# Kernel tuning notes

Hardware: AMD Instinct MI355X
Metric: run time of the kernel (lower is better)

The kernel has to match this reference:

```python
import jax, jax.numpy as jnp
import numpy as np

H, DH = 16, 64  # heads, dim_head (inner_dim = 1024)


def _sdpa(q, k, v):
    # q: (B, Q, D), k/v: (B, K, D); scale = 1/sqrt(D) as in F.scaled_dot_product_attention
    scale = 1.0 / jnp.sqrt(jnp.asarray(q.shape[-1], q.dtype))
    s = jnp.einsum('bqd,bkd->bqk', q, k) * scale
    return jnp.einsum('bqk,bkd->bqd', jax.nn.softmax(s, axis=-1), v)


def setup_inputs() -> dict:
    key = jax.random.key(0)
    ks = jax.random.split(key, 3)
    b, f, n, dim = 8, 16, 196, 1024
    N = 1 + f * n  # CLS + frames*patches = 3137
    x = jax.random.normal(ks[0], (b, N, dim), jnp.float32)
    w_qkv = jax.random.normal(ks[1], (3 * H * DH, dim), jnp.float32) * 0.02
    w_out = jax.random.normal(ks[2], (dim, H * DH), jnp.float32) * 0.02
    b_out = jnp.zeros((dim,), jnp.float32)
    return {"x": x, "w_qkv": w_qkv, "w_out": w_out, "b_out": b_out, "f": f}


def reference(x, w_qkv, w_out, b_out, f):
    b, N, dim = x.shape
    n = (N - 1) // f  # patches per frame

    qkv = x @ w_qkv.T  # (b, N, 3*H*DH)
    q, k, v = jnp.split(qkv, 3, axis=-1)

    def to_bh(t):  # 'b n (h d) -> (b h) n d'
        return t.reshape(b, N, H, DH).transpose(0, 2, 1, 3).reshape(b * H, N, DH)

    q, k, v = map(to_bh, (q, k, v))

    cls_q, q_ = q[:, :1], q[:, 1:]
    cls_k, k_ = k[:, :1], k[:, 1:]
    cls_v, v_ = v[:, :1], v[:, 1:]

    # CLS token attends over all tokens
    cls_out = _sdpa(cls_q, k, v)  # (b*H, 1, DH)

    # spatial attention: '(b h) (f n) d -> (b h f) n d'
    def to_space(t):
        return t.reshape(b * H, f, n, DH).reshape(b * H * f, n, DH)

    q_, k_, v_ = map(to_space, (q_, k_, v_))

    # repeat_interleave CLS k/v over the f groups, then prepend
    ck = jnp.repeat(cls_k, f, axis=0)  # (b*H*f, 1, DH)
    cv = jnp.repeat(cls_v, f, axis=0)
    k_ = jnp.concatenate((ck, k_), axis=1)  # (b*H*f, n+1, DH)
    v_ = jnp.concatenate((cv, v_), axis=1)

    out = _sdpa(q_, k_, v_)  # (b*H*f, n, DH)
    out = out.reshape(b * H, f * n, DH)  # '(b f) n d -> b (f n) d'
    out = jnp.concatenate((cls_out, out), axis=1)  # (b*H, N, DH)
    # '(b h) n d -> b n (h d)'
    out = out.reshape(b, H, N, DH).transpose(0, 2, 1, 3).reshape(b, N, H * DH)
    return out @ w_out.T + b_out
```

## Files before the change

kernel.cpp:

```cpp
#include <hip/hip_runtime.h>
#include <cstdint>
#include <cstddef>

#define DEVINL __device__ __forceinline__

typedef __attribute__((ext_vector_type(8))) short short8;
typedef __attribute__((ext_vector_type(4))) float f32x4;
typedef unsigned short u16;
typedef unsigned int u32;

DEVINL u16 f2b(float f) {
    u32 u = __float_as_uint(f);
    u32 r = (u + 0x7fffu + ((u >> 16) & 1u)) >> 16;
    return (u16)r;
}
DEVINL float b2f(u16 h) { return __uint_as_float(((u32)h) << 16); }

DEVINL void gl_lds16(const void* g, void* l) {
    __builtin_amdgcn_global_load_lds(
        (const __attribute__((address_space(1))) void*)g,
        (__attribute__((address_space(3))) void*)l, 16, 0, 0);
}

#define MROWS   25096
#define NTOK    3137
#define QE      25698304
#define LOG2E   1.4426950408889634f
#define SCL2    0.1803368801111204f

__global__ __launch_bounds__(256) void cvt_kernel(const float* __restrict__ in,
                                                  u16* __restrict__ out, int n4) {
    int i = blockIdx.x * blockDim.x + threadIdx.x;
    int stride = gridDim.x * blockDim.x;
    for (int j = i; j < n4; j += stride) {
        float4 v = ((const float4*)in)[j];
        ushort4 o;
        o.x = f2b(v.x); o.y = f2b(v.y); o.z = f2b(v.z); o.w = f2b(v.w);
        ((ushort4*)out)[j] = o;
    }
}


#define LDS_BUF 32768
#define NTILES  16

template <int MODE>
__global__ __launch_bounds__(512, 2) void gemm256(const u16* __restrict__ A,
                                                  const u16* __restrict__ B,
                                                  u16* __restrict__ q_out,
                                                  u16* __restrict__ k_out,
                                                  u16* __restrict__ v_out,
                                                  const float* __restrict__ bias,
                                                  float* __restrict__ f_out, int M) {
    __shared__ u16 lds[2 * LDS_BUF];
    const int tid = threadIdx.x, lane = tid & 63, w = tid >> 6;
    const int Mm1 = M - 1;

    const u32 nwg = gridDim.x * gridDim.y;
    const u32 orig = blockIdx.y * gridDim.x + blockIdx.x;
    const u32 q8 = nwg >> 3, r8 = nwg & 7, xcd = orig & 7, rest = orig >> 3;
    const u32 wg = (xcd < r8 ? xcd * (q8 + 1) : r8 * (q8 + 1) + (xcd - r8) * q8) + rest;
    const int m0 = (int)(wg / gridDim.x) * 256;
    const int n0 = (int)(wg % gridDim.x) * 256;

    const int wm = w >> 2, wn = w & 3;

    const int stRow = lane >> 2;
    const int stCol = (((lane & 3) ^ ((lane >> 3) & 3)) << 3);

    const int slotOff = (((lane >> 4) ^ ((lane >> 1) & 3)) << 3);
    const int rdA = (wm * 128 + (lane & 15)) * 32 + slotOff;
    const int rdB = (wn * 64 + (lane & 15)) * 32 + slotOff + 16384;

#define STAGE_A(NB, KK, KT) do {                                              \
    _Pragma("unroll") for (int j_ = 0; j_ < 2; ++j_) {                        \
        const int c_ = (w << 1) | j_;                                         \
        int r_ = m0 + c_ * 16 + stRow; if (r_ > Mm1) r_ = Mm1;                \
        gl_lds16(A + (size_t)r_ * 1024 + (KT) + (KK) * 32 + stCol,            \
                 lds + (NB) + (KK) * 8192 + c_ * 512);                        \
    } } while (0)

#define STAGE_B(NB, KK, KT) do {                                              \
    _Pragma("unroll") for (int j_ = 0; j_ < 2; ++j_) {                        \
        const int c_ = (w << 1) | j_;                                         \
        const int r_ = n0 + c_ * 16 + stRow;                                  \
        gl_lds16(B + (size_t)r_ * 1024 + (KT) + (KK) * 32 + stCol,            \
                 lds + (NB) + 16384 + (KK) * 8192 + c_ * 512);                \
    } } while (0)

#define LDA4(DST, CB, KK, MB) do {                                            \
    _Pragma("unroll") for (int i_ = 0; i_ < 4; ++i_)                          \
        DST[i_] = *(const short8*)&lds[(CB) + (KK) * 8192 + rdA +             \
                                       ((MB) + i_) * 16 * 32];                \
    } while (0)

#define LDB4(DST, CB, KK) do {                                                \
    _Pragma("unroll") for (int i_ = 0; i_ < 4; ++i_)                          \
        DST[i_] = *(const short8*)&lds[(CB) + (KK) * 8192 + rdB +             \
                                       i_ * 16 * 32];                         \
    } while (0)

#define MFMA16(AV, BV, MB) do {                                               \
    _Pragma("unroll") for (int i_ = 0; i_ < 4; ++i_)                          \
        _Pragma("unroll") for (int n_ = 0; n_ < 4; ++n_)                      \
            acc[(MB) + i_][n_] = __builtin_amdgcn_mfma_f32_16x16x32_bf16(     \
                AV[i_], BV[n_], acc[(MB) + i_][n_], 0, 0, 0);                 \
    } while (0)

#define PHASE_BAR() do {                                                      \
    __builtin_amdgcn_s_barrier();                                             \
    __builtin_amdgcn_sched_barrier(0); } while (0)

    f32x4 acc[8][4];
    const f32x4 zf = {0.f, 0.f, 0.f, 0.f};
#pragma unroll
    for (int i = 0; i < 8; ++i)
#pragma unroll
        for (int j = 0; j < 4; ++j) acc[i][j] = zf;

    STAGE_A(0, 0, 0);
    STAGE_B(0, 0, 0);
    STAGE_A(0, 1, 0);
    STAGE_B(0, 1, 0);
    asm volatile("s_waitcnt vmcnt(4)" ::: "memory");
    __builtin_amdgcn_sched_barrier(0);
    PHASE_BAR();

    for (int T = 0; T < NTILES; ++T) {
        const int cb = (T & 1) * LDS_BUF;
        const int nb = ((T + 1) & 1) * LDS_BUF;
        const bool pf = (T < NTILES - 1);
        const int kt1 = (T + 1) * 64;

        short8 a0m0[4], a0m4[4], a1m0[4], a1m4[4], b0[4], b1[4];

        LDA4(a0m0, cb, 0, 0);
        LDB4(b0,   cb, 0);
        LDA4(a0m4, cb, 0, 4);
        if (pf) STAGE_A(nb, 0, kt1);
        __builtin_amdgcn_s_setprio(1);
        MFMA16(a0m0, b0, 0);
        __builtin_amdgcn_s_setprio(0);
        if (pf) { asm volatile("s_waitcnt vmcnt(2)" ::: "memory"); }
        else    { asm volatile("s_waitcnt vmcnt(0)" ::: "memory"); }
        __builtin_amdgcn_sched_barrier(0);
        PHASE_BAR();

        LDA4(a1m0, cb, 1, 0);
        LDB4(b1,   cb, 1);
        if (pf) STAGE_B(nb, 0, kt1);
        __builtin_amdgcn_s_setprio(1);
        MFMA16(a0m4, b0, 4);
        __builtin_amdgcn_s_setprio(0);
        PHASE_BAR();

        LDA4(a1m4, cb, 1, 4);
        if (pf) STAGE_A(nb, 1, kt1);
        __builtin_amdgcn_s_setprio(1);
        MFMA16(a1m0, b1, 0);
        __builtin_amdgcn_s_setprio(0);
        PHASE_BAR();

        if (pf) STAGE_B(nb, 1, kt1);
        __builtin_amdgcn_s_setprio(1);
        MFMA16(a1m4, b1, 4);
        __builtin_amdgcn_s_setprio(0);
        if (pf) {
            asm volatile("s_waitcnt vmcnt(4)" ::: "memory");
            __builtin_amdgcn_sched_barrier(0);
        }
        PHASE_BAR();
    }

#pragma unroll
    for (int m = 0; m < 8; ++m) {
#pragma unroll
        for (int n = 0; n < 4; ++n) {
#pragma unroll
            for (int r = 0; r < 4; ++r) {
                const int gm = m0 + wm * 128 + m * 16 + ((lane >> 4) << 2) + r;
                if (gm < M) {
                    const int gc = n0 + wn * 64 + n * 16 + (lane & 15);
                    if (MODE == 0) {
                        const int t = gc >> 10;
                        const int h = (gc >> 6) & 15;
                        const int d = gc & 63;
                        const u32 bb = (u32)gm / 3137u;
                        const u32 nn = (u32)gm - bb * 3137u;
                        u16* dst = (t == 0) ? q_out : (t == 1) ? k_out : v_out;
                        dst[(((size_t)(bb * 16 + h)) * NTOK + nn) * 64 + d] =
                            f2b(acc[m][n][r]);
                    } else {
                        f_out[(size_t)gm * 1024 + gc] = acc[m][n][r] + bias[gc];
                    }
                }
            }
        }
    }
#undef STAGE_A
#undef STAGE_B
#undef LDA4
#undef LDB4
#undef MFMA16
#undef PHASE_BAR
}

#define CSZ 393
__global__ __launch_bounds__(256) void attn_cls_part(const u16* __restrict__ qb,
                                                     const u16* __restrict__ kb,
                                                     const u16* __restrict__ vb,
                                                     float* __restrict__ part) {
    const int bid = blockIdx.x;
    const int bh = bid >> 3, c = bid & 7;
    const size_t base = (size_t)bh * NTOK * 64;
    const int tid = threadIdx.x, lane = tid & 63, wid = tid >> 6;
    const int j0 = c * CSZ;
    const int cnt = min(NTOK - j0, CSZ);

    __shared__ float qs[64];
    __shared__ float sc[CSZ];
    __shared__ float redbuf[8];
    __shared__ float ored[4][64];

    if (tid < 64) qs[tid] = b2f(qb[base + tid]);
    __syncthreads();

    for (int j = tid; j < cnt; j += 256) {
        const u16* kr = kb + base + (size_t)(j0 + j) * 64;
        float acc = 0.f;
#pragma unroll
        for (int c2 = 0; c2 < 8; ++c2) {
            short8 v8 = *(const short8*)(kr + c2 * 8);
#pragma unroll
            for (int t = 0; t < 8; ++t) acc += qs[c2 * 8 + t] * b2f((u16)v8[t]);
        }
        sc[j] = acc * 0.125f;
    }
    __syncthreads();

    float mx = -1e30f;
    for (int j = tid; j < cnt; j += 256) mx = fmaxf(mx, sc[j]);
#pragma unroll
    for (int m = 32; m >= 1; m >>= 1) mx = fmaxf(mx, __shfl_xor(mx, m));
    if (lane == 0) redbuf[wid] = mx;
    __syncthreads();
    mx = fmaxf(fmaxf(redbuf[0], redbuf[1]), fmaxf(redbuf[2], redbuf[3]));

    float sum = 0.f;
    for (int j = tid; j < cnt; j += 256) {
        float p = exp2f((sc[j] - mx) * LOG2E);
        sc[j] = p;
        sum += p;
    }
#pragma unroll
    for (int m = 32; m >= 1; m >>= 1) sum += __shfl_xor(sum, m);
    if (lane == 0) redbuf[4 + wid] = sum;
    __syncthreads();
    const float tot = redbuf[4] + redbuf[5] + redbuf[6] + redbuf[7];

    const int d = tid & 63, g = tid >> 6;
    float o = 0.f;
    for (int j = g; j < cnt; j += 4)
        o += sc[j] * b2f(vb[base + (size_t)(j0 + j) * 64 + d]);
    ored[g][d] = o;
    __syncthreads();

    float* pb = part + (size_t)bid * 66;
    if (tid < 64) pb[2 + tid] = ored[0][tid] + ored[1][tid] + ored[2][tid] + ored[3][tid];
    else if (tid == 64) pb[0] = mx;
    else if (tid == 65) pb[1] = tot;
}

__global__ __launch_bounds__(64) void attn_cls_fin(const float* __restrict__ part,
                                                   u16* __restrict__ attnb) {
    const int bh = blockIdx.x, d = threadIdx.x;
    const int bb = bh >> 4, h = bh & 15;
    float m = -1e30f;
#pragma unroll
    for (int c = 0; c < 8; ++c) m = fmaxf(m, part[(size_t)(bh * 8 + c) * 66]);
    float t = 0.f, o = 0.f;
#pragma unroll
    for (int c = 0; c < 8; ++c) {
        const float* pb = part + (size_t)(bh * 8 + c) * 66;
        const float w = exp2f((pb[0] - m) * LOG2E);
        t += w * pb[1];
        o += w * pb[2 + d];
    }
    attnb[(size_t)bb * NTOK * 1024 + h * 64 + d] = f2b(o / t);
}

__global__ __launch_bounds__(256, 3) void attn_spatial(const u16* __restrict__ qb,
                                                       const u16* __restrict__ kb,
                                                       const u16* __restrict__ vb,
                                                       u16* __restrict__ attnb) {
    const int blk = blockIdx.x;
    const int bh = blk >> 4, fi = blk & 15;
    const int bb = bh >> 4, h = bh & 15;
    const int tid = threadIdx.x, lane = tid & 63, wid = tid >> 6;
    const int hi = lane >> 4, lo = lane & 15;
    const size_t kvbase = (size_t)bh * NTOK * 64;

    __shared__ u16 Kl[208 * 64];
    __shared__ u16 Vt[64 * 208];

    const short8 z8 = {0, 0, 0, 0, 0, 0, 0, 0};

    for (int idx = tid; idx < 208 * 8; idx += 256) {
        const int j = idx >> 3, c = idx & 7;
        short8 kval = z8;
        if (j < 197) {
            const int n = (j == 0) ? 0 : (1 + fi * 196 + (j - 1));
            kval = *(const short8*)(kb + kvbase + (size_t)n * 64 + c * 8);
            const short8 v8 = *(const short8*)(vb + kvbase + (size_t)n * 64 + c * 8);
#pragma unroll
            for (int t0 = 0; t0 < 8; ++t0) {
                const int t = (t0 + c) & 7;
                Vt[(c * 8 + t) * 208 + j] = (u16)v8[t];
            }
        } else {
#pragma unroll
            for (int t = 0; t < 8; ++t) Vt[(c * 8 + t) * 208 + j] = 0;
        }
        *(short8*)(Kl + ((j * 64 + c * 8) ^ ((j & 7) << 3))) = kval;
    }
    __syncthreads();

    const int ksw = (lo & 7) << 3;
    const int src0 = lo + ((hi & 1) << 5);
    const int src1 = src0 + 16;
    const f32x4 zf = {0.f, 0.f, 0.f, 0.f};

    for (int mf = wid; mf < 13; mf += 4) {
        int qr = mf * 16 + lo; if (qr > 195) qr = 195;
        const u16* qp = qb + kvbase + (size_t)(1 + fi * 196 + qr) * 64 + hi * 8;
        const short8 qb0 = *(const short8*)(qp);
        const short8 qb1 = *(const short8*)(qp + 32);

        f32x4 s[13];
#pragma unroll
        for (int nf = 0; nf < 13; ++nf) s[nf] = zf;
#pragma unroll
        for (int nf = 0; nf < 13; ++nf) {
            const int e0 = (nf * 16 + lo) * 64 + hi * 8;
            const short8 a0 = *(const short8*)(Kl + (e0 ^ ksw));
            const short8 a1 = *(const short8*)(Kl + ((e0 + 32) ^ ksw));
            s[nf] = __builtin_amdgcn_mfma_f32_16x16x32_bf16(a0, qb0, s[nf], 0, 0, 0);
            s[nf] = __builtin_amdgcn_mfma_f32_16x16x32_bf16(a1, qb1, s[nf], 0, 0, 0);
        }

        float mx = s[0][0];
#pragma unroll
        for (int nf = 0; nf < 13; ++nf)
#pragma unroll
            for (int reg = 0; reg < 4; ++reg) mx = fmaxf(mx, s[nf][reg]);
        mx = fmaxf(mx, __shfl_xor(mx, 16));
        mx = fmaxf(mx, __shfl_xor(mx, 32));
        const float mC = mx * SCL2;
        float sum = 0.f;
#pragma unroll
        for (int nf = 0; nf < 13; ++nf)
#pragma unroll
            for (int reg = 0; reg < 4; ++reg) {
                const float p = exp2f(fmaf(s[nf][reg], SCL2, -mC));
                s[nf][reg] = p;
                sum += p;
            }
        sum += __shfl_xor(sum, 16);
        sum += __shfl_xor(sum, 32);
        const float rls = 1.0f / (sum - 11.0f * exp2f(-mC));

        u32 w0[13], w1[13];
#pragma unroll
        for (int nf = 0; nf < 13; ++nf) {
            const float p0 = s[nf][0] * rls, p1 = s[nf][1] * rls;
            const float p2 = s[nf][2] * rls, p3 = s[nf][3] * rls;
            asm("v_cvt_pk_bf16_f32 %0, %1, %2" : "=v"(w0[nf]) : "v"(p0), "v"(p1));
            asm("v_cvt_pk_bf16_f32 %0, %1, %2" : "=v"(w1[nf]) : "v"(p2), "v"(p3));
        }

        f32x4 o[4];
#pragma unroll
        for (int i = 0; i < 4; ++i) o[i] = zf;
#pragma unroll
        for (int kk = 0; kk < 7; ++kk) {
            u32 x0, x1, x2, x3;
            if (kk < 6) {
                const u32 aA0 = __shfl(w0[2 * kk], src0), aA1 = __shfl(w1[2 * kk], src0);
                const u32 aA2 = __shfl(w0[2 * kk], src1), aA3 = __shfl(w1[2 * kk], src1);
                const u32 aB0 = __shfl(w0[2 * kk + 1], src0), aB1 = __shfl(w1[2 * kk + 1], src0);
                const u32 aB2 = __shfl(w0[2 * kk + 1], src1), aB3 = __shfl(w1[2 * kk + 1], src1);
                const bool lh = hi < 2;
                x0 = lh ? aA0 : aB0; x1 = lh ? aA1 : aB1;
                x2 = lh ? aA2 : aB2; x3 = lh ? aA3 : aB3;
            } else {
                const u32 aA0 = __shfl(w0[12], src0), aA1 = __shfl(w1[12], src0);
                const u32 aA2 = __shfl(w0[12], src1), aA3 = __shfl(w1[12], src1);
                const bool lh = hi < 2;
                x0 = lh ? aA0 : 0u; x1 = lh ? aA1 : 0u;
                x2 = lh ? aA2 : 0u; x3 = lh ? aA3 : 0u;
            }
            union { u32 u[4]; short8 v; } pu;
            pu.u[0] = x0; pu.u[1] = x1; pu.u[2] = x2; pu.u[3] = x3;
            const short8 pa = pu.v;
#pragma unroll
            for (int nf2 = 0; nf2 < 4; ++nf2) {
                short8 bv = z8;
                if (kk < 6 || hi < 2)
                    bv = *(const short8*)(Vt + (nf2 * 16 + lo) * 208 + kk * 32 + hi * 8);
                o[nf2] = __builtin_amdgcn_mfma_f32_16x16x32_bf16(pa, bv, o[nf2], 0, 0, 0);
            }
        }

#pragma unroll
        for (int nf2 = 0; nf2 < 4; ++nf2)
#pragma unroll
            for (int reg = 0; reg < 4; ++reg) {
                const int r = mf * 16 + hi * 4 + reg;
                if (r < 196) {
                    const int d = nf2 * 16 + lo;
                    const size_t nn = 1 + fi * 196 + r;
                    attnb[((size_t)bb * NTOK + nn) * 1024 + h * 64 + d] =
                        f2b(o[nf2][reg]);
                }
            }
    }
}

extern "C" void kernel_launch(void* const* d_in, const int* in_sizes, int n_in,
                              void* d_out, int out_size, void* d_ws, size_t ws_size,
                              hipStream_t stream) {
    const float* x = (const float*)d_in[0];
    const float* w_qkv = (const float*)d_in[1];
    const float* w_out = (const float*)d_in[2];
    const float* b_out = (const float*)d_in[3];

    const size_t need = ((size_t)QE * 2 + 3145728 + 1048576) * 2;
    if (ws_size < need) {
        hipMemsetAsync(d_out, 0, (size_t)out_size * 4, stream);
        return;
    }

    u16* vb = (u16*)d_ws;
    u16* xab = vb + QE;
    u16* wqb = xab + QE;
    u16* wob = wqb + 3145728;
    u16* qb = (u16*)d_out;
    u16* kb = qb + QE;
    float* outf = (float*)d_out;
    float* clsp = (float*)wqb;

    cvt_kernel<<<2048, 256, 0, stream>>>(x, xab, QE / 4);
    cvt_kernel<<<2048, 256, 0, stream>>>(w_qkv, wqb, 3145728 / 4);
    cvt_kernel<<<1024, 256, 0, stream>>>(w_out, wob, 1048576 / 4);

    gemm256<0><<<dim3(12, 99), 512, 0, stream>>>(xab, wqb, qb, kb, vb, nullptr,
                                                 nullptr, MROWS);
    attn_cls_part<<<1024, 256, 0, stream>>>(qb, kb, vb, clsp);
    attn_cls_fin<<<128, 64, 0, stream>>>(clsp, xab);
    attn_spatial<<<2048, 256, 0, stream>>>(qb, kb, vb, xab);
    gemm256<1><<<dim3(4, 99), 512, 0, stream>>>(xab, wob, nullptr, nullptr, nullptr,
                                                b_out, outf, MROWS);
}
```

Measured before the change: 449.4 us.

## Prefetch next tile's first LDS fragments in GEMM loop and defer softmax normalization

In the GEMM main loop, the first A/B fragments of the next K-tile are loaded from LDS during the last phase of the current tile. The first MFMA block of each iteration then no longer waits on LDS reads, and the vmcnt waits move to match. In the spatial attention kernel, unnormalized probabilities are packed to bf16 and the 1/sum factor is applied to the output after PV, fetched per row via shuffle. This removes per-element multiplies before conversion but changes bf16 rounding slightly and adds register pressure in the GEMM.

```diff
diff --git a/kernel.cpp b/kernel.cpp
--- a/kernel.cpp
+++ b/kernel.cpp
@@ -107,6 +107,10 @@
                 AV[i_], BV[n_], acc[(MB) + i_][n_], 0, 0, 0);                 \
     } while (0)
 
+#define VMW(N) do {                                                           \
+    asm volatile("s_waitcnt vmcnt(" #N ")" ::: "memory");                     \
+    __builtin_amdgcn_sched_barrier(0); } while (0)
+
 #define PHASE_BAR() do {                                                      \
     __builtin_amdgcn_s_barrier();                                             \
     __builtin_amdgcn_sched_barrier(0); } while (0)
@@ -122,9 +126,12 @@
     STAGE_B(0, 0, 0);
     STAGE_A(0, 1, 0);
     STAGE_B(0, 1, 0);
-    asm volatile("s_waitcnt vmcnt(4)" ::: "memory");
-    __builtin_amdgcn_sched_barrier(0);
+    VMW(4);
     PHASE_BAR();
+
+    short8 ra[4], rb[4];
+    LDA4(ra, 0, 0, 0);
+    LDB4(rb, 0, 0);
 
     for (int T = 0; T < NTILES; ++T) {
         const int cb = (T & 1) * LDS_BUF;
@@ -132,43 +139,41 @@
         const bool pf = (T < NTILES - 1);
         const int kt1 = (T + 1) * 64;
 
-        short8 a0m0[4], a0m4[4], a1m0[4], a1m4[4], b0[4], b1[4];
-
-        LDA4(a0m0, cb, 0, 0);
-        LDB4(b0,   cb, 0);
-        LDA4(a0m4, cb, 0, 4);
+        short8 a4[4], c0[4], d0[4], e4[4];
+
+        LDA4(a4, cb, 0, 4);
         if (pf) STAGE_A(nb, 0, kt1);
         __builtin_amdgcn_s_setprio(1);
-        MFMA16(a0m0, b0, 0);
+        MFMA16(ra, rb, 0);
         __builtin_amdgcn_s_setprio(0);
-        if (pf) { asm volatile("s_waitcnt vmcnt(2)" ::: "memory"); }
-        else    { asm volatile("s_waitcnt vmcnt(0)" ::: "memory"); }
-        __builtin_amdgcn_sched_barrier(0);
+        if (pf) { VMW(2); }
+        else    { VMW(0); }
         PHASE_BAR();
 
-        LDA4(a1m0, cb, 1, 0);
-        LDB4(b1,   cb, 1);
+        LDA4(c0, cb, 1, 0);
+        LDB4(d0, cb, 1);
         if (pf) STAGE_B(nb, 0, kt1);
         __builtin_amdgcn_s_setprio(1);
-        MFMA16(a0m4, b0, 4);
+        MFMA16(a4, rb, 4);
         __builtin_amdgcn_s_setprio(0);
         PHASE_BAR();
 
-        LDA4(a1m4, cb, 1, 4);
+        LDA4(e4, cb, 1, 4);
         if (pf) STAGE_A(nb, 1, kt1);
         __builtin_amdgcn_s_setprio(1);
-        MFMA16(a1m0, b1, 0);
+        MFMA16(c0, d0, 0);
         __builtin_amdgcn_s_setprio(0);
+        if (pf) { VMW(2); }
         PHASE_BAR();
 
-        if (pf) STAGE_B(nb, 1, kt1);
+        if (pf) {
+            LDA4(ra, nb, 0, 0);
+            LDB4(rb, nb, 0);
+            STAGE_B(nb, 1, kt1);
+        }
         __builtin_amdgcn_s_setprio(1);
-        MFMA16(a1m4, b1, 4);
+        MFMA16(e4, d0, 4);
         __builtin_amdgcn_s_setprio(0);
-        if (pf) {
-            asm volatile("s_waitcnt vmcnt(4)" ::: "memory");
-            __builtin_amdgcn_sched_barrier(0);
-        }
         PHASE_BAR();
     }
 
@@ -202,6 +207,7 @@
 #undef LDA4
 #undef LDB4
 #undef MFMA16
+#undef VMW
 #undef PHASE_BAR
 }
 
@@ -372,10 +378,10 @@
         u32 w0[13], w1[13];
 #pragma unroll
         for (int nf = 0; nf < 13; ++nf) {
-            const float p0 = s[nf][0] * rls, p1 = s[nf][1] * rls;
-            const float p2 = s[nf][2] * rls, p3 = s[nf][3] * rls;
-            asm("v_cvt_pk_bf16_f32 %0, %1, %2" : "=v"(w0[nf]) : "v"(p0), "v"(p1));
-            asm("v_cvt_pk_bf16_f32 %0, %1, %2" : "=v"(w1[nf]) : "v"(p2), "v"(p3));
+            asm("v_cvt_pk_bf16_f32 %0, %1, %2"
+                : "=v"(w0[nf]) : "v"(s[nf][0]), "v"(s[nf][1]));
+            asm("v_cvt_pk_bf16_f32 %0, %1, %2"
+                : "=v"(w1[nf]) : "v"(s[nf][2]), "v"(s[nf][3]));
         }
 
         f32x4 o[4];
@@ -411,6 +417,9 @@
             }
         }
 
+        float rr[4];
+#pragma unroll
+        for (int reg = 0; reg < 4; ++reg) rr[reg] = __shfl(rls, hi * 4 + reg);
 #pragma unroll
         for (int nf2 = 0; nf2 < 4; ++nf2)
 #pragma unroll
@@ -420,7 +429,7 @@
                     const int d = nf2 * 16 + lo;
                     const size_t nn = 1 + fi * 196 + r;
                     attnb[((size_t)bb * NTOK + nn) * 1024 + h * 64 + d] =
-                        f2b(o[nf2][reg]);
+                        f2b(o[nf2][reg] * rr[reg]);
                 }
             }
     }
```

After: 447.6 us (median of 3 runs). Within noise of the previous version (-0.4%).
